# Performance work log

Measured on AMD Instinct MI355X. Metric: run time of the kernel, lower is better.

## Reference

```python
import jax, jax.numpy as jnp
import numpy as np

N = 1024      # number of atoms
L = 64        # latent_size
VOCAB = 20    # vocab_size (len(ATOM_CATEGORIES))


def _lin(key, fan_in, fan_out):
    # mimic torch nn.Linear init: U(-1/sqrt(fan_in), 1/sqrt(fan_in))
    kw, kb = jax.random.split(key)
    s = 1.0 / np.sqrt(fan_in)
    W = jax.random.uniform(kw, (fan_in, fan_out), minval=-s, maxval=s, dtype=jnp.float32)
    b = jax.random.uniform(kb, (fan_out,), minval=-s, maxval=s, dtype=jnp.float32)
    return W, b


def setup_inputs() -> dict:
    key = jax.random.key(0)
    ks = jax.random.split(key, 9)
    We1, be1 = _lin(ks[3], 2 * L + 1, L)   # mlp_e layer 1
    We2, be2 = _lin(ks[4], L, L)           # mlp_e layer 2
    Wh1, bh1 = _lin(ks[5], L + 1, L)       # mlp_h layer 1
    Wh2, bh2 = _lin(ks[6], L, L)           # mlp_h layer 2
    Wo, bo = _lin(ks[7], L, 1)             # output_mlp
    return {
        "atom_categories": jax.random.randint(ks[0], (N,), 0, VOCAB),
        "atom_coordinates": jax.random.normal(ks[1], (N, 3), dtype=jnp.float32),
        "learnable_matrix": jax.random.normal(ks[2], (VOCAB, L), dtype=jnp.float32),
        "We1": We1, "be1": be1, "We2": We2, "be2": be2,
        "Wh1": Wh1, "bh1": bh1, "Wh2": Wh2, "bh2": bh2,
        "Wo": Wo, "bo": bo,
    }


def reference(atom_categories, atom_coordinates, learnable_matrix,
              We1, be1, We2, be2, Wh1, bh1, Wh2, bh2, Wo, bo):
    Z = atom_coordinates
    # init_H: learnable_matrix.T @ one_hot(cat) == row gather
    H = learnable_matrix[atom_categories]                       # [N, L]

    # pairwise squared distances ||Z_i - Z_j||^2
    d2 = jnp.sum((Z[:, None, :] - Z[None, :, :]) ** 2, axis=-1)  # [N, N]

    # mlp_e layer 1 on concat(H_i, H_j, d2): split We1 to avoid materializing concat
    W1i, W1j, w1z = We1[:L], We1[L:2 * L], We1[2 * L]            # [L,L],[L,L],[L]
    pre_i = H @ W1i                                              # [N, L]
    pre_j = H @ W1j                                              # [N, L]
    h1 = jnp.tanh(pre_i[:, None, :] + pre_j[None, :, :]
                  + d2[:, :, None] * w1z + be1)                  # [N, N, L]
    W_e = jnp.tanh(h1 @ We2 + be2)                               # [N, N, L]

    # V[i] = sum over j != i of sum_l W_e[i,j,l]
    total = jnp.sum(W_e, axis=(1, 2))                            # [N]
    diag = jnp.einsum('iil->i', W_e)                             # [N]
    V = total - diag                                             # [N]

    # mlp_h on concat(H_i, V_i): split Wh1
    hh = jnp.tanh(H @ Wh1[:L] + V[:, None] * Wh1[L] + bh1)       # [N, L]
    newH = jnp.tanh(hh @ Wh2 + bh2)                              # [N, L]

    Hsum = jnp.sum(newH, axis=0)                                 # [L]
    return (Hsum @ Wo + bo)[0]                                   # scalar
```

## Files before the change

kernel.cpp:

```cpp
#include <hip/hip_runtime.h>
#include <hip/hip_bf16.h>


#define N_ATOMS 1024
#define L_DIM 64
#define CSCALE 2.8853900817779268f
#define T2LD 68

typedef _Float16 f16x8 __attribute__((ext_vector_type(8)));
typedef __fp16  fp16x2 __attribute__((ext_vector_type(2)));
typedef float f32x4 __attribute__((ext_vector_type(4)));

__device__ __forceinline__ float tanh_fast(float x) {
    float e = __builtin_amdgcn_exp2f(x * CSCALE);
    float r = __builtin_amdgcn_rcpf(e + 1.0f);
    return fmaf(-2.0f, r, 1.0f);
}

__global__ __launch_bounds__(256) void k_one(const int* __restrict__ cat,
                                             const float* __restrict__ Z,
                                             const float* __restrict__ LM,
                                             const float* __restrict__ We1,
                                             const float* __restrict__ be1,
                                             const float* __restrict__ We2,
                                             const float* __restrict__ be2,
                                             const float* __restrict__ Wh1,
                                             const float* __restrict__ bh1,
                                             const float* __restrict__ Wh2,
                                             const float* __restrict__ bh2,
                                             const float* __restrict__ Wo,
                                             const float* __restrict__ bo,
                                             float* __restrict__ out) {
    int i = blockIdx.x;
    int t = threadIdx.x;
    int lane = t & 63;
    int wave = t >> 6;
    int nlo = lane & 15;
    int quad = lane >> 4;

    __shared__ __align__(16) float d2s[N_ATOMS];
    __shared__ int   cats[N_ATOMS];
    __shared__ __align__(16) float LMs[20 * L_DIM];
    __shared__ __align__(16) float T2s[20 * T2LD];
    __shared__ __align__(16) float preIs[L_DIM];
    __shared__ float red[256];
    __shared__ f16x8 bLs[8 * 64];
    __shared__ float dgt[L_DIM];
    __shared__ float hhs[L_DIM];

    float zi0 = Z[i * 3], zi1 = Z[i * 3 + 1], zi2 = Z[i * 3 + 2];
    for (int p = t; p < N_ATOMS; p += 256) {
        cats[p] = cat[p];
        float a = zi0 - Z[p * 3], b = zi1 - Z[p * 3 + 1], c = zi2 - Z[p * 3 + 2];
        d2s[p] = a * a + b * b + c * c;
    }
    for (int p = t; p < 20 * L_DIM; p += 256) LMs[p] = LM[p];
    __syncthreads();

    {
        float a0 = 0.f, a1 = 0.f, a2 = 0.f, a3 = 0.f, a4 = 0.f;
#pragma unroll 16
        for (int m = 0; m < L_DIM; m++) {
            float w = We1[(L_DIM + m) * L_DIM + lane];
            a0 = fmaf(LMs[(wave +  0) * L_DIM + m], w, a0);
            a1 = fmaf(LMs[(wave +  4) * L_DIM + m], w, a1);
            a2 = fmaf(LMs[(wave +  8) * L_DIM + m], w, a2);
            a3 = fmaf(LMs[(wave + 12) * L_DIM + m], w, a3);
            a4 = fmaf(LMs[(wave + 16) * L_DIM + m], w, a4);
        }
        float b = be1[lane];
        T2s[(wave +  0) * T2LD + lane] = (a0 + b) * CSCALE;
        T2s[(wave +  4) * T2LD + lane] = (a1 + b) * CSCALE;
        T2s[(wave +  8) * T2LD + lane] = (a2 + b) * CSCALE;
        T2s[(wave + 12) * T2LD + lane] = (a3 + b) * CSCALE;
        T2s[(wave + 16) * T2LD + lane] = (a4 + b) * CSCALE;
    }
    int ci = cats[i];
    if (wave == 0) {
        float s = 0.f;
#pragma unroll 16
        for (int m = 0; m < L_DIM; m++)
            s = fmaf(LMs[ci * L_DIM + m], We1[m * L_DIM + lane], s);
        preIs[lane] = s * CSCALE;
    }

    f16x8 bH[4][2];
    float biasR[4];
#pragma unroll
    for (int nt = 0; nt < 4; nt++) {
        float psum = 0.f;
#pragma unroll
        for (int kt = 0; kt < 2; kt++) {
            f16x8 hi8, lo8;
#pragma unroll
            for (int e = 0; e < 8; e++) {
                float x = We2[(kt * 32 + quad * 8 + e) * L_DIM + nt * 16 + nlo];
                psum += x;
                float wp = -2.0f * CSCALE * x;
                _Float16 hi = (_Float16)wp;
                hi8[e] = hi;
                lo8[e] = (_Float16)(wp - (float)hi);
            }
            bH[nt][kt] = hi8;
            if (wave == 0) bLs[(kt * 4 + nt) * 64 + lane] = lo8;
        }
        psum += __shfl_xor(psum, 16);
        psum += __shfl_xor(psum, 32);
        biasR[nt] = CSCALE * (be2[nt * 16 + nlo] + psum);
    }

    int mbs[4];
    f32x4 wzR[4];
#pragma unroll
    for (int g = 0; g < 4; g++) {
        int mb = ((g >> 1) << 5) + (quad << 3) + ((g & 1) << 2);
        mbs[g] = mb;
        f32x4 wz = *(const f32x4*)(We1 + 2 * L_DIM * L_DIM + mb);
        wzR[g] = wz * CSCALE;
    }

    __syncthreads();

    f32x4 aiR[4];
#pragma unroll
    for (int g = 0; g < 4; g++) aiR[g] = *(const f32x4*)(preIs + mbs[g]);

    int sc0 = cats[(wave * 16 + 0) * 16 + nlo];
    const float* Tr0 = T2s + sc0 * T2LD;
    f32x4 p0 = *(const f32x4*)(Tr0 + mbs[0]) + aiR[0];
    f32x4 p1 = *(const f32x4*)(Tr0 + mbs[1]) + aiR[1];
    f32x4 p2 = *(const f32x4*)(Tr0 + mbs[2]) + aiR[2];
    f32x4 p3 = *(const f32x4*)(Tr0 + mbs[3]) + aiR[3];

    f32x4 Vr4 = {0.f, 0.f, 0.f, 0.f};
    for (int k = 0; k < 16; k++) {
        float d2 = d2s[(wave * 16 + k) * 16 + nlo];
        f32x4 d2v = {d2, d2, d2, d2};

        f32x4 z0 = p0 + d2v * wzR[0];
        f32x4 z1 = p1 + d2v * wzR[1];
        f32x4 z2 = p2 + d2v * wzR[2];
        f32x4 z3 = p3 + d2v * wzR[3];
        f32x4 ex0, ex1, ex2, ex3;
#pragma unroll
        for (int e = 0; e < 4; e++) {
            ex0[e] = __builtin_amdgcn_exp2f(z0[e]);
            ex1[e] = __builtin_amdgcn_exp2f(z1[e]);
            ex2[e] = __builtin_amdgcn_exp2f(z2[e]);
            ex3[e] = __builtin_amdgcn_exp2f(z3[e]);
        }
        ex0 += 1.0f; ex1 += 1.0f; ex2 += 1.0f; ex3 += 1.0f;
        f32x4 r0, r1, r2, r3;
#pragma unroll
        for (int e = 0; e < 4; e++) {
            r0[e] = __builtin_amdgcn_rcpf(ex0[e]);
            r1[e] = __builtin_amdgcn_rcpf(ex1[e]);
            r2[e] = __builtin_amdgcn_rcpf(ex2[e]);
            r3[e] = __builtin_amdgcn_rcpf(ex3[e]);
        }
        union { f16x8 v; fp16x2 h2[4]; } u0, u1;
        u0.h2[0] = __builtin_amdgcn_cvt_pkrtz(r0[0], r0[1]);
        u0.h2[1] = __builtin_amdgcn_cvt_pkrtz(r0[2], r0[3]);
        u0.h2[2] = __builtin_amdgcn_cvt_pkrtz(r1[0], r1[1]);
        u0.h2[3] = __builtin_amdgcn_cvt_pkrtz(r1[2], r1[3]);
        u1.h2[0] = __builtin_amdgcn_cvt_pkrtz(r2[0], r2[1]);
        u1.h2[1] = __builtin_amdgcn_cvt_pkrtz(r2[2], r2[3]);
        u1.h2[2] = __builtin_amdgcn_cvt_pkrtz(r3[0], r3[1]);
        u1.h2[3] = __builtin_amdgcn_cvt_pkrtz(r3[2], r3[3]);
        f16x8 aH0 = u0.v, aH1 = u1.v;

        if (k < 15) {
            int sc = cats[(wave * 16 + k + 1) * 16 + nlo];
            const float* Tr = T2s + sc * T2LD;
            p0 = *(const f32x4*)(Tr + mbs[0]) + aiR[0];
            p1 = *(const f32x4*)(Tr + mbs[1]) + aiR[1];
            p2 = *(const f32x4*)(Tr + mbs[2]) + aiR[2];
            p3 = *(const f32x4*)(Tr + mbs[3]) + aiR[3];
        }

#pragma unroll
        for (int nt = 0; nt < 4; nt++) {
            f16x8 bl0 = bLs[(0 * 4 + nt) * 64 + lane];
            f16x8 bl1 = bLs[(1 * 4 + nt) * 64 + lane];
            f32x4 acc = {biasR[nt], biasR[nt], biasR[nt], biasR[nt]};
            acc = __builtin_amdgcn_mfma_f32_16x16x32_f16(aH0, bH[nt][0], acc, 0, 0, 0);
            acc = __builtin_amdgcn_mfma_f32_16x16x32_f16(aH0, bl0, acc, 0, 0, 0);
            acc = __builtin_amdgcn_mfma_f32_16x16x32_f16(aH1, bH[nt][1], acc, 0, 0, 0);
            acc = __builtin_amdgcn_mfma_f32_16x16x32_f16(aH1, bl1, acc, 0, 0, 0);
            f32x4 ev;
#pragma unroll
            for (int r4 = 0; r4 < 4; r4++) ev[r4] = __builtin_amdgcn_exp2f(acc[r4]);
            ev += 1.0f;
            f32x4 rv;
#pragma unroll
            for (int r4 = 0; r4 < 4; r4++) rv[r4] = __builtin_amdgcn_rcpf(ev[r4]);
            Vr4 += rv;
        }
    }

    red[t] = Vr4[0] + Vr4[1] + Vr4[2] + Vr4[3];
    __syncthreads();

    float Rall;
    if (t < 64) {
        float r = red[t] + red[t + 64] + red[t + 128] + red[t + 192];
#pragma unroll
        for (int o = 32; o > 0; o >>= 1) r += __shfl_xor(r, o);
        Rall = r;
        float z = preIs[t] + T2s[ci * T2LD + t];
        float rr = __builtin_amdgcn_rcpf(__builtin_amdgcn_exp2f(z) + 1.0f);
        dgt[t] = fmaf(-2.0f, rr, 1.0f);
    }
    __syncthreads();
    if (t < 64) {
        float S = be2[t];
#pragma unroll
        for (int m = 0; m < L_DIM; m++) S = fmaf(dgt[m], We2[m * L_DIM + t], S);
        float rd = __builtin_amdgcn_rcpf(__builtin_amdgcn_exp2f(S * CSCALE) + 1.0f);
#pragma unroll
        for (int o = 32; o > 0; o >>= 1) rd += __shfl_xor(rd, o);
        float V = fmaf(-2.0f, Rall - rd, (float)(1023 * L_DIM));
        float s = 0.f;
#pragma unroll
        for (int m = 0; m < L_DIM; m++) s = fmaf(LMs[ci * L_DIM + m], Wh1[m * L_DIM + t], s);
        s = fmaf(V, Wh1[L_DIM * L_DIM + t], s) + bh1[t];
        hhs[t] = tanh_fast(s);
    }
    __syncthreads();
    if (t < 64) {
        float s2 = 0.f;
#pragma unroll
        for (int m = 0; m < L_DIM; m++) s2 = fmaf(hhs[m], Wh2[m * L_DIM + t], s2);
        float nh = tanh_fast(s2 + bh2[t]);
        float w = nh * Wo[t];
#pragma unroll
        for (int o = 32; o > 0; o >>= 1) w += __shfl_down(w, o);
        if (t == 0) atomicAdd(out, w + (i == 0 ? bo[0] : 0.f));
    }
}

extern "C" void kernel_launch(void* const* d_in, const int* in_sizes, int n_in,
                              void* d_out, int out_size, void* d_ws, size_t ws_size,
                              hipStream_t stream) {
    const int*   cat = (const int*)  d_in[0];
    const float* Z   = (const float*)d_in[1];
    const float* LM  = (const float*)d_in[2];
    const float* We1 = (const float*)d_in[3];
    const float* be1 = (const float*)d_in[4];
    const float* We2 = (const float*)d_in[5];
    const float* be2 = (const float*)d_in[6];
    const float* Wh1 = (const float*)d_in[7];
    const float* bh1 = (const float*)d_in[8];
    const float* Wh2 = (const float*)d_in[9];
    const float* bh2 = (const float*)d_in[10];
    const float* Wo  = (const float*)d_in[11];
    const float* bo  = (const float*)d_in[12];
    float* out = (float*)d_out;

    k_one<<<N_ATOMS, 256, 0, stream>>>(cat, Z, LM, We1, be1, We2, be2,
                                       Wh1, bh1, Wh2, bh2, Wo, bo, out);
}
```

Before: 129.8 us.

## Split pair loop across two blocks per atom and move tail MLP to second kernel

The main kernel now launches two blocks per atom, each covering half of the j range, which doubles the grid and halves the per-block serial loop. Partial sums and the diagonal pre-activation are written to workspace. A second kernel then finishes the per-atom MLP, packing four atoms per block. This takes the serial single-wave tail out of the main kernel, at the cost of a second launch and recomputing the per-block setup (T2 table, gathers) twice per atom.

```diff
diff --git a/kernel.cpp b/kernel.cpp
--- a/kernel.cpp
+++ b/kernel.cpp
@@ -17,44 +17,40 @@
     return fmaf(-2.0f, r, 1.0f);
 }
 
-__global__ __launch_bounds__(256) void k_one(const int* __restrict__ cat,
-                                             const float* __restrict__ Z,
-                                             const float* __restrict__ LM,
-                                             const float* __restrict__ We1,
-                                             const float* __restrict__ be1,
-                                             const float* __restrict__ We2,
-                                             const float* __restrict__ be2,
-                                             const float* __restrict__ Wh1,
-                                             const float* __restrict__ bh1,
-                                             const float* __restrict__ Wh2,
-                                             const float* __restrict__ bh2,
-                                             const float* __restrict__ Wo,
-                                             const float* __restrict__ bo,
-                                             float* __restrict__ out) {
-    int i = blockIdx.x;
+__global__ __launch_bounds__(256) void k_main(const int* __restrict__ cat,
+                                              const float* __restrict__ Z,
+                                              const float* __restrict__ LM,
+                                              const float* __restrict__ We1,
+                                              const float* __restrict__ be1,
+                                              const float* __restrict__ We2,
+                                              const float* __restrict__ be2,
+                                              float* __restrict__ Vhalf,
+                                              float* __restrict__ diagz) {
+    int bid = blockIdx.x;
+    int i = bid >> 1, half = bid & 1;
     int t = threadIdx.x;
     int lane = t & 63;
     int wave = t >> 6;
     int nlo = lane & 15;
     int quad = lane >> 4;
 
-    __shared__ __align__(16) float d2s[N_ATOMS];
-    __shared__ int   cats[N_ATOMS];
+    __shared__ __align__(16) float d2s[512];
+    __shared__ int   cats[512];
     __shared__ __align__(16) float LMs[20 * L_DIM];
     __shared__ __align__(16) float T2s[20 * T2LD];
     __shared__ __align__(16) float preIs[L_DIM];
     __shared__ float red[256];
     __shared__ f16x8 bLs[8 * 64];
-    __shared__ float dgt[L_DIM];
-    __shared__ float hhs[L_DIM];
 
     float zi0 = Z[i * 3], zi1 = Z[i * 3 + 1], zi2 = Z[i * 3 + 2];
-    for (int p = t; p < N_ATOMS; p += 256) {
-        cats[p] = cat[p];
-        float a = zi0 - Z[p * 3], b = zi1 - Z[p * 3 + 1], c = zi2 - Z[p * 3 + 2];
+    for (int p = t; p < 512; p += 256) {
+        int j = half * 512 + p;
+        cats[p] = cat[j];
+        float a = zi0 - Z[j * 3], b = zi1 - Z[j * 3 + 1], c = zi2 - Z[j * 3 + 2];
         d2s[p] = a * a + b * b + c * c;
     }
     for (int p = t; p < 20 * L_DIM; p += 256) LMs[p] = LM[p];
+    int ci = cat[i];
     __syncthreads();
 
     {
@@ -75,7 +71,6 @@
         T2s[(wave + 12) * T2LD + lane] = (a3 + b) * CSCALE;
         T2s[(wave + 16) * T2LD + lane] = (a4 + b) * CSCALE;
     }
-    int ci = cats[i];
     if (wave == 0) {
         float s = 0.f;
 #pragma unroll 16
@@ -125,7 +120,7 @@
 #pragma unroll
     for (int g = 0; g < 4; g++) aiR[g] = *(const f32x4*)(preIs + mbs[g]);
 
-    int sc0 = cats[(wave * 16 + 0) * 16 + nlo];
+    int sc0 = cats[nlo + wave * 128];
     const float* Tr0 = T2s + sc0 * T2LD;
     f32x4 p0 = *(const f32x4*)(Tr0 + mbs[0]) + aiR[0];
     f32x4 p1 = *(const f32x4*)(Tr0 + mbs[1]) + aiR[1];
@@ -133,8 +128,8 @@
     f32x4 p3 = *(const f32x4*)(Tr0 + mbs[3]) + aiR[3];
 
     f32x4 Vr4 = {0.f, 0.f, 0.f, 0.f};
-    for (int k = 0; k < 16; k++) {
-        float d2 = d2s[(wave * 16 + k) * 16 + nlo];
+    for (int k = 0; k < 8; k++) {
+        float d2 = d2s[(wave * 8 + k) * 16 + nlo];
         f32x4 d2v = {d2, d2, d2, d2};
 
         f32x4 z0 = p0 + d2v * wzR[0];
@@ -169,8 +164,8 @@
         u1.h2[3] = __builtin_amdgcn_cvt_pkrtz(r3[2], r3[3]);
         f16x8 aH0 = u0.v, aH1 = u1.v;
 
-        if (k < 15) {
-            int sc = cats[(wave * 16 + k + 1) * 16 + nlo];
+        if (k < 7) {
+            int sc = cats[(wave * 8 + k + 1) * 16 + nlo];
             const float* Tr = T2s + sc * T2LD;
             p0 = *(const f32x4*)(Tr + mbs[0]) + aiR[0];
             p1 = *(const f32x4*)(Tr + mbs[1]) + aiR[1];
@@ -201,42 +196,64 @@
     red[t] = Vr4[0] + Vr4[1] + Vr4[2] + Vr4[3];
     __syncthreads();
 
-    float Rall;
     if (t < 64) {
         float r = red[t] + red[t + 64] + red[t + 128] + red[t + 192];
 #pragma unroll
         for (int o = 32; o > 0; o >>= 1) r += __shfl_xor(r, o);
-        Rall = r;
-        float z = preIs[t] + T2s[ci * T2LD + t];
-        float rr = __builtin_amdgcn_rcpf(__builtin_amdgcn_exp2f(z) + 1.0f);
-        dgt[t] = fmaf(-2.0f, rr, 1.0f);
-    }
-    __syncthreads();
-    if (t < 64) {
-        float S = be2[t];
-#pragma unroll
-        for (int m = 0; m < L_DIM; m++) S = fmaf(dgt[m], We2[m * L_DIM + t], S);
-        float rd = __builtin_amdgcn_rcpf(__builtin_amdgcn_exp2f(S * CSCALE) + 1.0f);
-#pragma unroll
-        for (int o = 32; o > 0; o >>= 1) rd += __shfl_xor(rd, o);
-        float V = fmaf(-2.0f, Rall - rd, (float)(1023 * L_DIM));
-        float s = 0.f;
-#pragma unroll
-        for (int m = 0; m < L_DIM; m++) s = fmaf(LMs[ci * L_DIM + m], Wh1[m * L_DIM + t], s);
-        s = fmaf(V, Wh1[L_DIM * L_DIM + t], s) + bh1[t];
-        hhs[t] = tanh_fast(s);
-    }
-    __syncthreads();
-    if (t < 64) {
-        float s2 = 0.f;
-#pragma unroll
-        for (int m = 0; m < L_DIM; m++) s2 = fmaf(hhs[m], Wh2[m * L_DIM + t], s2);
-        float nh = tanh_fast(s2 + bh2[t]);
-        float w = nh * Wo[t];
-#pragma unroll
-        for (int o = 32; o > 0; o >>= 1) w += __shfl_down(w, o);
-        if (t == 0) atomicAdd(out, w + (i == 0 ? bo[0] : 0.f));
-    }
+        if (half == 0) diagz[i * L_DIM + t] = preIs[t] + T2s[ci * T2LD + t];
+        if (t == 0) Vhalf[bid] = r;
+    }
+}
+
+__global__ __launch_bounds__(256) void k_post(const int* __restrict__ cat,
+                                              const float* __restrict__ LM,
+                                              const float* __restrict__ We2,
+                                              const float* __restrict__ be2,
+                                              const float* __restrict__ Wh1,
+                                              const float* __restrict__ bh1,
+                                              const float* __restrict__ Wh2,
+                                              const float* __restrict__ bh2,
+                                              const float* __restrict__ Wo,
+                                              const float* __restrict__ bo,
+                                              const float* __restrict__ Vhalf,
+                                              const float* __restrict__ diagz,
+                                              float* __restrict__ out) {
+    int t = threadIdx.x;
+    int sub = t >> 6, lane = t & 63;
+    int i = blockIdx.x * 4 + sub;
+    __shared__ float dgt[4][L_DIM];
+    __shared__ float hrow_s[4][L_DIM];
+    __shared__ float hh_s[4][L_DIM];
+
+    float Rall = Vhalf[2 * i] + Vhalf[2 * i + 1];
+    float z = diagz[i * L_DIM + lane];
+    float rr = __builtin_amdgcn_rcpf(__builtin_amdgcn_exp2f(z) + 1.0f);
+    dgt[sub][lane] = fmaf(-2.0f, rr, 1.0f);
+    hrow_s[sub][lane] = LM[cat[i] * L_DIM + lane];
+    __syncthreads();
+
+    float S = be2[lane];
+#pragma unroll
+    for (int m = 0; m < L_DIM; m++) S = fmaf(dgt[sub][m], We2[m * L_DIM + lane], S);
+    float rd = __builtin_amdgcn_rcpf(__builtin_amdgcn_exp2f(S * CSCALE) + 1.0f);
+#pragma unroll
+    for (int o = 32; o > 0; o >>= 1) rd += __shfl_xor(rd, o);
+    float V = fmaf(-2.0f, Rall - rd, (float)(1023 * L_DIM));
+    float s = 0.f;
+#pragma unroll
+    for (int m = 0; m < L_DIM; m++) s = fmaf(hrow_s[sub][m], Wh1[m * L_DIM + lane], s);
+    s = fmaf(V, Wh1[L_DIM * L_DIM + lane], s) + bh1[lane];
+    hh_s[sub][lane] = tanh_fast(s);
+    __syncthreads();
+
+    float s2 = 0.f;
+#pragma unroll
+    for (int m = 0; m < L_DIM; m++) s2 = fmaf(hh_s[sub][m], Wh2[m * L_DIM + lane], s2);
+    float nh = tanh_fast(s2 + bh2[lane]);
+    float w = nh * Wo[lane];
+#pragma unroll
+    for (int o = 32; o > 0; o >>= 1) w += __shfl_down(w, o);
+    if (lane == 0) atomicAdd(out, w + (i == 0 ? bo[0] : 0.f));
 }
 
 extern "C" void kernel_launch(void* const* d_in, const int* in_sizes, int n_in,
@@ -257,6 +274,13 @@
     const float* bo  = (const float*)d_in[12];
     float* out = (float*)d_out;
 
-    k_one<<<N_ATOMS, 256, 0, stream>>>(cat, Z, LM, We1, be1, We2, be2,
-                                       Wh1, bh1, Wh2, bh2, Wo, bo, out);
-}
+    float* ws    = (float*)d_ws;
+    float* diagz = ws;
+    float* Vhalf = diagz + N_ATOMS * L_DIM;
+
+    k_main<<<N_ATOMS * 2, 256, 0, stream>>>(cat, Z, LM, We1, be1, We2, be2,
+                                            Vhalf, diagz);
+    k_post<<<N_ATOMS / 4, 256, 0, stream>>>(cat, LM, We2, be2,
+                                            Wh1, bh1, Wh2, bh2, Wo, bo,
+                                            Vhalf, diagz, out);
+}
```

New measurement: 150.0 us. 15.6% more time.
